# Kernel tuning notes

Hardware: AMD Instinct MI355X
Metric: run time of the kernel (lower is better)

The kernel has to match this reference:

```python
import jax, jax.numpy as jnp
import numpy as np

N, D, H = 8192, 512, 8
HD = D // H  # head_dim = 64


def setup_inputs() -> dict:
    key = jax.random.key(0)
    ks = jax.random.split(key, 9)
    s = 0.02
    return {
        "x": jax.random.normal(ks[0], (N, D), dtype=jnp.float32),
        "Wq": jax.random.normal(ks[1], (H, D, HD), dtype=jnp.float32) * s,
        "bq": jax.random.normal(ks[2], (H, HD), dtype=jnp.float32) * s,
        "Wk": jax.random.normal(ks[3], (H, D, HD), dtype=jnp.float32) * s,
        "bk": jax.random.normal(ks[4], (H, HD), dtype=jnp.float32) * s,
        "Wv": jax.random.normal(ks[5], (H, D, HD), dtype=jnp.float32) * s,
        "bv": jax.random.normal(ks[6], (H, HD), dtype=jnp.float32) * s,
        "Wo": jax.random.normal(ks[7], (D, D), dtype=jnp.float32) * s,
        "bo": jax.random.normal(ks[8], (D,), dtype=jnp.float32) * s,
    }


def reference(x, Wq, bq, Wk, bk, Wv, bv, Wo, bo):
    # Per-head linear projections (batched over heads): [H, N, HD]
    q = jnp.einsum("nd,hde->hne", x, Wq) + bq[:, None, :]
    k = jnp.einsum("nd,hde->hne", x, Wk) + bk[:, None, :]
    v = jnp.einsum("nd,hde->hne", x, Wv) + bv[:, None, :]
    scale = 1.0 / jnp.sqrt(jnp.float32(HD))
    # Global attention over all N points: scores [H, N, N]
    scores = jnp.einsum("hne,hme->hnm", q, k) * scale
    attn = jax.nn.softmax(scores, axis=-1)
    heads = jnp.einsum("hnm,hme->hne", attn, v)  # [H, N, HD]
    # Concat heads -> [N, D]
    concat = jnp.transpose(heads, (1, 0, 2)).reshape(N, D)
    out = concat @ Wo + bo
    return out + x
```

## Files before the change

kernel.cpp:

```cpp
#include <hip/hip_runtime.h>
#include <hip/hip_bf16.h>

#define NPTS 8192
#define DIM  512
#define NHEAD 8
#define HDIM 64

typedef short bf16x8 __attribute__((ext_vector_type(8)));
typedef float f32x4  __attribute__((ext_vector_type(4)));

#define GLOBAL_AS __attribute__((address_space(1)))
#define LDS_AS    __attribute__((address_space(3)))

#if __has_builtin(__builtin_amdgcn_exp2f)
#define EXP2F(x) __builtin_amdgcn_exp2f(x)
#else
#define EXP2F(x) __expf((x) * 0.6931471805599453f)
#endif

__device__ __forceinline__ unsigned short f2bf(float f) {
    union { float f; unsigned int u; } v; v.f = f;
    unsigned int r = v.u + 0x7FFFu + ((v.u >> 16) & 1u);
    return (unsigned short)(r >> 16);
}
__device__ __forceinline__ float bf2f(unsigned short u) {
    union { unsigned int i; float f; } v; v.i = ((unsigned int)u) << 16;
    return v.f;
}
__device__ __forceinline__ unsigned int pk2bf(float a, float b) {
    __hip_bfloat162 h = __float22bfloat162_rn(float2{a, b});
    union { __hip_bfloat162 h; unsigned int u; } v; v.h = h;
    return v.u;
}

__global__ __launch_bounds__(256) void cvt_x_kernel(
    const float* __restrict__ in, unsigned short* __restrict__ outp)
{
    int gid = blockIdx.x * 256 + threadIdx.x;
    float4 a = ((const float4*)in)[gid * 2];
    float4 b = ((const float4*)in)[gid * 2 + 1];
    uint4 u;
    u.x = pk2bf(a.x, a.y); u.y = pk2bf(a.z, a.w);
    u.z = pk2bf(b.x, b.y); u.w = pk2bf(b.z, b.w);
    ((uint4*)outp)[gid] = u;
}

__global__ __launch_bounds__(256) void tr_w_kernel(
    const float* __restrict__ Wq, const float* __restrict__ Wk,
    const float* __restrict__ Wv, unsigned short* __restrict__ wtq)
{
    int zh = blockIdx.z, z = zh >> 3, h = zh & 7;
    const float* src = (z == 0 ? Wq : z == 1 ? Wk : Wv) + (size_t)h * DIM * HDIM;
    unsigned short* dst = wtq + (size_t)zh * HDIM * DIM;
    int k0 = blockIdx.x * 64;
    __shared__ float tile[64][65];
    int t = threadIdx.x, c = t & 63, r = t >> 6;
    #pragma unroll
    for (int i = 0; i < 16; ++i)
        tile[r + 4 * i][c] = src[(size_t)(k0 + r + 4 * i) * HDIM + c];
    __syncthreads();
    #pragma unroll
    for (int i = 0; i < 16; ++i)
        dst[(size_t)(r + 4 * i) * DIM + k0 + c] = f2bf(tile[c][r + 4 * i]);
}

__global__ __launch_bounds__(256) void tr_wo_kernel(
    const float* __restrict__ Wo, unsigned short* __restrict__ wot)
{
    int k0 = blockIdx.x * 64, e0 = blockIdx.y * 64;
    __shared__ float tile[64][65];
    int t = threadIdx.x, c = t & 63, r = t >> 6;
    #pragma unroll
    for (int i = 0; i < 16; ++i)
        tile[r + 4 * i][c] = Wo[(size_t)(k0 + r + 4 * i) * DIM + e0 + c];
    __syncthreads();
    #pragma unroll
    for (int i = 0; i < 16; ++i)
        wot[(size_t)(e0 + r + 4 * i) * DIM + k0 + c] = f2bf(tile[c][r + 4 * i]);
}

__global__ __launch_bounds__(256) void qkv_mfma_kernel(
    const unsigned short* __restrict__ xbf,
    const unsigned short* __restrict__ wtq,
    const float* __restrict__ bq, const float* __restrict__ bk,
    const float* __restrict__ bv,
    unsigned short* __restrict__ q_bf, unsigned short* __restrict__ k_bf,
    unsigned short* __restrict__ vt_bf)
{
    const int zh = blockIdx.y, z = zh >> 3, h = zh & 7;
    const unsigned short* W = wtq + (size_t)zh * HDIM * DIM;
    const float* b = (z == 0 ? bq : z == 1 ? bk : bv) + h * HDIM;
    const int t = threadIdx.x, w = t >> 6, lane = t & 63;
    const int l15 = lane & 15, quad = lane >> 4;
    const int r0 = blockIdx.x * 128 + w * 32;

    __shared__ __align__(16) unsigned short Wlds[2][64 * 64];

    const int koff0 = l15 * 64 + (quad ^ (l15 & 7)) * 8;
    const int koff1 = koff0 ^ 32;
    const int srow   = lane >> 3;
    const int schunk = (lane & 7) ^ srow;

    const unsigned short* Wp = W + (size_t)(16 * w + srow) * DIM + schunk * 8;

    __builtin_amdgcn_global_load_lds((const GLOBAL_AS void*)Wp,
        (LDS_AS void*)&Wlds[0][(16 * w) * 64], 16, 0, 0);
    __builtin_amdgcn_global_load_lds((const GLOBAL_AS void*)(Wp + (size_t)8 * DIM),
        (LDS_AS void*)&Wlds[0][(16 * w + 8) * 64], 16, 0, 0);
    Wp += 64;
    __syncthreads();
    int buf = 0;

    f32x4 O[2][4];
    #pragma unroll
    for (int mt = 0; mt < 2; ++mt)
        #pragma unroll
        for (int tn = 0; tn < 4; ++tn) O[mt][tn] = (f32x4){0.f, 0.f, 0.f, 0.f};

    for (int k0 = 0; k0 < DIM; k0 += 64) {
        if (k0 + 64 < DIM) {
            int nb = buf ^ 1;
            __builtin_amdgcn_global_load_lds((const GLOBAL_AS void*)Wp,
                (LDS_AS void*)&Wlds[nb][(16 * w) * 64], 16, 0, 0);
            __builtin_amdgcn_global_load_lds(
                (const GLOBAL_AS void*)(Wp + (size_t)8 * DIM),
                (LDS_AS void*)&Wlds[nb][(16 * w + 8) * 64], 16, 0, 0);
            Wp += 64;
        }

        bf16x8 af[2][2];
        #pragma unroll
        for (int mt = 0; mt < 2; ++mt)
            #pragma unroll
            for (int kc = 0; kc < 2; ++kc)
                af[mt][kc] = *(const bf16x8*)
                    &xbf[(size_t)(r0 + 16 * mt + l15) * DIM + k0 + quad * 8 + 32 * kc];

        bf16x8 bf[4][2];
        #pragma unroll
        for (int tn = 0; tn < 4; ++tn) {
            bf[tn][0] = *(const bf16x8*)&Wlds[buf][1024 * tn + koff0];
            bf[tn][1] = *(const bf16x8*)&Wlds[buf][1024 * tn + koff1];
        }

        #pragma unroll
        for (int mt = 0; mt < 2; ++mt)
            #pragma unroll
            for (int tn = 0; tn < 4; ++tn) {
                O[mt][tn] = __builtin_amdgcn_mfma_f32_16x16x32_bf16(
                    af[mt][0], bf[tn][0], O[mt][tn], 0, 0, 0);
                O[mt][tn] = __builtin_amdgcn_mfma_f32_16x16x32_bf16(
                    af[mt][1], bf[tn][1], O[mt][tn], 0, 0, 0);
            }

        __syncthreads();
        buf ^= 1;
    }

    if (z < 2) {
        unsigned short* outp = (z == 0 ? q_bf : k_bf) + (size_t)h * NPTS * HDIM;
        const float sc = (z == 0) ? 0.18033688011112042f : 1.0f;
        #pragma unroll
        for (int mt = 0; mt < 2; ++mt)
            #pragma unroll
            for (int tn = 0; tn < 4; ++tn) {
                int e = l15 + 16 * tn;
                float be = b[e];
                #pragma unroll
                for (int r = 0; r < 4; ++r) {
                    int n = r0 + 16 * mt + quad * 4 + r;
                    outp[(size_t)n * HDIM + e] = f2bf((O[mt][tn][r] + be) * sc);
                }
            }
    } else {
        unsigned short* vt = vt_bf + (size_t)h * HDIM * NPTS;
        #pragma unroll
        for (int mt = 0; mt < 2; ++mt)
            #pragma unroll
            for (int tn = 0; tn < 4; ++tn) {
                int e = l15 + 16 * tn;
                float be = b[e];
                uint2 pk;
                pk.x = pk2bf(O[mt][tn][0] + be, O[mt][tn][1] + be);
                pk.y = pk2bf(O[mt][tn][2] + be, O[mt][tn][3] + be);
                *(uint2*)&vt[(size_t)e * NPTS + r0 + quad * 8 + mt * 4] = pk;
            }
    }
}

#define STAGE_TILE(B)                                                         \
    do {                                                                      \
        __builtin_amdgcn_global_load_lds((const GLOBAL_AS void*)Kp,           \
            (LDS_AS void*)&Klds[B][(16 * w) * 64], 16, 0, 0);                 \
        __builtin_amdgcn_global_load_lds((const GLOBAL_AS void*)(Kp + 8 * HDIM), \
            (LDS_AS void*)&Klds[B][(16 * w + 8) * 64], 16, 0, 0);             \
        __builtin_amdgcn_global_load_lds((const GLOBAL_AS void*)Vp0,          \
            (LDS_AS void*)&Vlds[B][(16 * w) * 64], 16, 0, 0);                 \
        __builtin_amdgcn_global_load_lds((const GLOBAL_AS void*)Vp1,          \
            (LDS_AS void*)&Vlds[B][(16 * w + 8) * 64], 16, 0, 0);             \
        Kp += 64 * HDIM; Vp0 += 64; Vp1 += 64;                                \
    } while (0)

__global__ __launch_bounds__(256) void attn_kernel(
    const unsigned short* __restrict__ qg,
    const unsigned short* __restrict__ kg,
    const unsigned short* __restrict__ vtg,
    unsigned short* __restrict__ opart,
    float* __restrict__ lpart)
{
    const int h  = blockIdx.y;
    const int ks = blockIdx.z;
    const int q0 = blockIdx.x * 256;
    const int kbase = ks * (NPTS / 2);
    const unsigned short* Q  = qg  + (size_t)h * NPTS * HDIM;
    const unsigned short* K  = kg  + (size_t)h * NPTS * HDIM;
    const unsigned short* Vt = vtg + (size_t)h * HDIM * NPTS;
    unsigned short* op = opart + (size_t)ks * NPTS * DIM;
    float* lp = lpart + (size_t)(ks * NHEAD + h) * NPTS;

    __shared__ __align__(16) unsigned short Klds[2][64 * 64];
    __shared__ __align__(16) unsigned short Vlds[2][64 * 64];

    const int t    = threadIdx.x;
    const int w    = t >> 6;
    const int lane = t & 63;
    const int l15  = lane & 15;
    const int quad = lane >> 4;

    const int koff0 = l15 * 64 + (quad ^ (l15 & 7)) * 8;
    const int koff1 = koff0 ^ 32;

    const int srow   = lane >> 3;
    const int schunk = (lane & 7) ^ srow;

    bf16x8 qf[4][2];
    #pragma unroll
    for (int m = 0; m < 4; ++m)
        #pragma unroll
        for (int kc = 0; kc < 2; ++kc)
            qf[m][kc] = *(const bf16x8*)
                &Q[(size_t)(q0 + 64 * w + 16 * m + l15) * HDIM + quad * 8 + 32 * kc];

    const bf16x8 ones = {(short)0x3F80, (short)0x3F80, (short)0x3F80,
                         (short)0x3F80, (short)0x3F80, (short)0x3F80,
                         (short)0x3F80, (short)0x3F80};
    const f32x4 Z0 = (f32x4){0.f, 0.f, 0.f, 0.f};

    f32x4 OT[4][4];
    f32x4 Lacc[4];
    #pragma unroll
    for (int te = 0; te < 4; ++te)
        #pragma unroll
        for (int m = 0; m < 4; ++m) OT[te][m] = (f32x4){0.f, 0.f, 0.f, 0.f};
    #pragma unroll
    for (int m = 0; m < 4; ++m) Lacc[m] = (f32x4){0.f, 0.f, 0.f, 0.f};

    const unsigned short* Kp  = K  + (size_t)(kbase + 16 * w + srow) * HDIM
                                   + schunk * 8;
    const unsigned short* Vp0 = Vt + (size_t)(16 * w + srow) * NPTS
                                   + kbase + schunk * 8;
    const unsigned short* Vp1 = Vp0 + (size_t)8 * NPTS;

    STAGE_TILE(0);
    __syncthreads();
    int buf = 0;

    for (int kt = 0; kt < NPTS / 2; kt += 64) {
        if (kt + 64 < NPTS / 2) {
            const int nxt = buf ^ 1;
            if (nxt) STAGE_TILE(1); else STAGE_TILE(0);
        }

        bf16x8 pt[2][4];

        {
            bf16x8 kf[2][2];
            #pragma unroll
            for (int kn = 0; kn < 2; ++kn) {
                kf[kn][0] = *(const bf16x8*)&Klds[buf][1024 * kn + koff0];
                kf[kn][1] = *(const bf16x8*)&Klds[buf][1024 * kn + koff1];
            }
            f32x4 st[2][4];
            #pragma unroll
            for (int kn = 0; kn < 2; ++kn)
                #pragma unroll
                for (int m = 0; m < 4; ++m) {
                    st[kn][m] = __builtin_amdgcn_mfma_f32_16x16x32_bf16(
                        kf[kn][0], qf[m][0], Z0, 0, 0, 0);
                    st[kn][m] = __builtin_amdgcn_mfma_f32_16x16x32_bf16(
                        kf[kn][1], qf[m][1], st[kn][m], 0, 0, 0);
                }
            #pragma unroll
            for (int m = 0; m < 4; ++m) {
                float e0 = EXP2F(st[0][m][0]);
                float e1 = EXP2F(st[0][m][1]);
                float e2 = EXP2F(st[0][m][2]);
                float e3 = EXP2F(st[0][m][3]);
                float e4 = EXP2F(st[1][m][0]);
                float e5 = EXP2F(st[1][m][1]);
                float e6 = EXP2F(st[1][m][2]);
                float e7 = EXP2F(st[1][m][3]);
                union { uint4 u; bf16x8 v; } uu;
                uu.u.x = pk2bf(e0, e1);
                uu.u.y = pk2bf(e2, e3);
                uu.u.z = pk2bf(e4, e5);
                uu.u.w = pk2bf(e6, e7);
                pt[0][m] = uu.v;
            }
        }

        bf16x8 vf0[2][2];
        #pragma unroll
        for (int te = 0; te < 2; ++te) {
            vf0[te][0] = *(const bf16x8*)&Vlds[buf][1024 * te + koff0];
            vf0[te][1] = *(const bf16x8*)&Vlds[buf][1024 * te + koff1];
        }

        {
            bf16x8 kf[2][2];
            #pragma unroll
            for (int kn = 0; kn < 2; ++kn) {
                kf[kn][0] = *(const bf16x8*)&Klds[buf][1024 * (kn + 2) + koff0];
                kf[kn][1] = *(const bf16x8*)&Klds[buf][1024 * (kn + 2) + koff1];
            }
            f32x4 st[2][4];
            #pragma unroll
            for (int kn = 0; kn < 2; ++kn)
                #pragma unroll
                for (int m = 0; m < 4; ++m) {
                    st[kn][m] = __builtin_amdgcn_mfma_f32_16x16x32_bf16(
                        kf[kn][0], qf[m][0], Z0, 0, 0, 0);
                    st[kn][m] = __builtin_amdgcn_mfma_f32_16x16x32_bf16(
                        kf[kn][1], qf[m][1], st[kn][m], 0, 0, 0);
                }
            #pragma unroll
            for (int m = 0; m < 4; ++m) {
                float e0 = EXP2F(st[0][m][0]);
                float e1 = EXP2F(st[0][m][1]);
                float e2 = EXP2F(st[0][m][2]);
                float e3 = EXP2F(st[0][m][3]);
                float e4 = EXP2F(st[1][m][0]);
                float e5 = EXP2F(st[1][m][1]);
                float e6 = EXP2F(st[1][m][2]);
                float e7 = EXP2F(st[1][m][3]);
                union { uint4 u; bf16x8 v; } uu;
                uu.u.x = pk2bf(e0, e1);
                uu.u.y = pk2bf(e2, e3);
                uu.u.z = pk2bf(e4, e5);
                uu.u.w = pk2bf(e6, e7);
                pt[1][m] = uu.v;
            }
        }

        bf16x8 vf1[2][2];
        #pragma unroll
        for (int te = 0; te < 2; ++te) {
            vf1[te][0] = *(const bf16x8*)&Vlds[buf][1024 * (te + 2) + koff0];
            vf1[te][1] = *(const bf16x8*)&Vlds[buf][1024 * (te + 2) + koff1];
        }

        #pragma unroll
        for (int kb = 0; kb < 2; ++kb)
            #pragma unroll
            for (int m = 0; m < 4; ++m)
                Lacc[m] = __builtin_amdgcn_mfma_f32_16x16x32_bf16(
                    ones, pt[kb][m], Lacc[m], 0, 0, 0);

        #pragma unroll
        for (int te = 0; te < 2; ++te)
            #pragma unroll
            for (int m = 0; m < 4; ++m) {
                OT[te][m] = __builtin_amdgcn_mfma_f32_16x16x32_bf16(
                    vf0[te][0], pt[0][m], OT[te][m], 0, 0, 0);
                OT[te][m] = __builtin_amdgcn_mfma_f32_16x16x32_bf16(
                    vf0[te][1], pt[1][m], OT[te][m], 0, 0, 0);
            }
        #pragma unroll
        for (int te = 0; te < 2; ++te)
            #pragma unroll
            for (int m = 0; m < 4; ++m) {
                OT[te + 2][m] = __builtin_amdgcn_mfma_f32_16x16x32_bf16(
                    vf1[te][0], pt[0][m], OT[te + 2][m], 0, 0, 0);
                OT[te + 2][m] = __builtin_amdgcn_mfma_f32_16x16x32_bf16(
                    vf1[te][1], pt[1][m], OT[te + 2][m], 0, 0, 0);
            }

        __syncthreads();
        buf ^= 1;
    }

    #pragma unroll
    for (int m = 0; m < 4; ++m) {
        int n = q0 + 64 * w + 16 * m + l15;
        if (quad == 0) lp[n] = Lacc[m][0];
        #pragma unroll
        for (int te = 0; te < 4; ++te) {
            uint2 pk;
            pk.x = pk2bf(OT[te][m][0], OT[te][m][1]);
            pk.y = pk2bf(OT[te][m][2], OT[te][m][3]);
            *(uint2*)&op[(size_t)n * DIM + h * HDIM + 16 * te + quad * 4] = pk;
        }
    }
}

__global__ __launch_bounds__(256) void reduce_kernel(
    unsigned short* __restrict__ op0, const unsigned short* __restrict__ op1,
    const float* __restrict__ l0, const float* __restrict__ l1)
{
    int gid = blockIdx.x * 256 + threadIdx.x;
    int n  = gid >> 7;
    int c4 = gid & 127;
    int h  = c4 >> 4;
    float inv = 1.0f / (l0[h * NPTS + n] + l1[h * NPTS + n]);
    ushort4 a = *(const ushort4*)&op0[(size_t)gid * 4];
    ushort4 b = *(const ushort4*)&op1[(size_t)gid * 4];
    uint2 o;
    o.x = pk2bf((bf2f(a.x) + bf2f(b.x)) * inv, (bf2f(a.y) + bf2f(b.y)) * inv);
    o.y = pk2bf((bf2f(a.z) + bf2f(b.z)) * inv, (bf2f(a.w) + bf2f(b.w)) * inv);
    *(uint2*)&op0[(size_t)gid * 4] = o;
}

__global__ __launch_bounds__(256) void out_mfma_kernel(
    const unsigned short* __restrict__ cc,
    const unsigned short* __restrict__ wot,
    const float* __restrict__ bo, const float* __restrict__ x,
    float* __restrict__ outp)
{
    const int t = threadIdx.x, w = t >> 6, lane = t & 63;
    const int l15 = lane & 15, quad = lane >> 4;
    const int r0 = blockIdx.x * 128 + w * 32;
    const int c0 = blockIdx.y * 64;

    f32x4 O[2][4];
    #pragma unroll
    for (int mt = 0; mt < 2; ++mt)
        #pragma unroll
        for (int tn = 0; tn < 4; ++tn) O[mt][tn] = (f32x4){0.f, 0.f, 0.f, 0.f};

    for (int k0 = 0; k0 < DIM; k0 += 64) {
        bf16x8 af[2][2], bf[4][2];
        #pragma unroll
        for (int mt = 0; mt < 2; ++mt)
            #pragma unroll
            for (int kc = 0; kc < 2; ++kc)
                af[mt][kc] = *(const bf16x8*)
                    &cc[(size_t)(r0 + 16 * mt + l15) * DIM + k0 + quad * 8 + 32 * kc];
        #pragma unroll
        for (int tn = 0; tn < 4; ++tn)
            #pragma unroll
            for (int kc = 0; kc < 2; ++kc)
                bf[tn][kc] = *(const bf16x8*)
                    &wot[(size_t)(c0 + l15 + 16 * tn) * DIM + k0 + quad * 8 + 32 * kc];
        #pragma unroll
        for (int mt = 0; mt < 2; ++mt)
            #pragma unroll
            for (int tn = 0; tn < 4; ++tn) {
                O[mt][tn] = __builtin_amdgcn_mfma_f32_16x16x32_bf16(
                    af[mt][0], bf[tn][0], O[mt][tn], 0, 0, 0);
                O[mt][tn] = __builtin_amdgcn_mfma_f32_16x16x32_bf16(
                    af[mt][1], bf[tn][1], O[mt][tn], 0, 0, 0);
            }
    }

    #pragma unroll
    for (int mt = 0; mt < 2; ++mt)
        #pragma unroll
        for (int tn = 0; tn < 4; ++tn) {
            int e = c0 + l15 + 16 * tn;
            float be = bo[e];
            #pragma unroll
            for (int r = 0; r < 4; ++r) {
                int n = r0 + 16 * mt + quad * 4 + r;
                outp[(size_t)n * DIM + e] = O[mt][tn][r] + be + x[(size_t)n * DIM + e];
            }
        }
}

extern "C" void kernel_launch(void* const* d_in, const int* in_sizes, int n_in,
                              void* d_out, int out_size, void* d_ws, size_t ws_size,
                              hipStream_t stream) {
    const float* x  = (const float*)d_in[0];
    const float* Wq = (const float*)d_in[1];
    const float* bq = (const float*)d_in[2];
    const float* Wk = (const float*)d_in[3];
    const float* bk = (const float*)d_in[4];
    const float* Wv = (const float*)d_in[5];
    const float* bv = (const float*)d_in[6];
    const float* Wo = (const float*)d_in[7];
    const float* bo = (const float*)d_in[8];
    float* out = (float*)d_out;

    const size_t per = (size_t)NHEAD * NPTS * HDIM;
    unsigned short* xbf   = (unsigned short*)d_ws;
    unsigned short* wtq   = xbf + (size_t)NPTS * DIM;
    unsigned short* wot   = wtq + (size_t)24 * HDIM * DIM;
    unsigned short* q_bf  = wot + (size_t)DIM * DIM;
    unsigned short* k_bf  = q_bf + per;
    unsigned short* vt_bf = k_bf + per;
    unsigned short* op0   = vt_bf + per;
    unsigned short* op1   = op0 + (size_t)NPTS * DIM;
    float*          lpart = (float*)(op1 + (size_t)NPTS * DIM);

    cvt_x_kernel<<<dim3(NPTS * DIM / 8 / 256), 256, 0, stream>>>(x, xbf);
    tr_w_kernel<<<dim3(8, 1, 24), 256, 0, stream>>>(Wq, Wk, Wv, wtq);
    tr_wo_kernel<<<dim3(8, 8), 256, 0, stream>>>(Wo, wot);
    qkv_mfma_kernel<<<dim3(NPTS / 128, 24), 256, 0, stream>>>(
        xbf, wtq, bq, bk, bv, q_bf, k_bf, vt_bf);
    attn_kernel<<<dim3(NPTS / 256, NHEAD, 2), 256, 0, stream>>>(
        q_bf, k_bf, vt_bf, op0, lpart);
    reduce_kernel<<<dim3(NPTS * DIM / 4 / 256), 256, 0, stream>>>(
        op0, op1, lpart, lpart + (size_t)NHEAD * NPTS);
    out_mfma_kernel<<<dim3(NPTS / 128, DIM / 64), 256, 0, stream>>>(
        op0, wot, bo, x, out);
}
```

Baseline: 295.8 us.

## Fuse split-KV reduction into output projection and stage Wo tiles in LDS

Removes the separate reduce kernel that merged the two split-KV partial outputs and normalized by the softmax denominators. The output projection kernel now loads both partials, runs MFMAs on each into a per-head temporary, and scales by 1/(l0+l1) before accumulating. This works because each 64-wide k-block corresponds to one head. Wo tiles are also double-buffered into swizzled LDS via global_load_lds instead of read directly from global memory by every wave. In exchange the MFMA count in the projection doubles, and op0/op1 are each read 8 times across column blocks.

```diff
diff --git a/kernel.cpp b/kernel.cpp
--- a/kernel.cpp
+++ b/kernel.cpp
@@ -403,25 +403,11 @@
     }
 }
 
-__global__ __launch_bounds__(256) void reduce_kernel(
-    unsigned short* __restrict__ op0, const unsigned short* __restrict__ op1,
-    const float* __restrict__ l0, const float* __restrict__ l1)
-{
-    int gid = blockIdx.x * 256 + threadIdx.x;
-    int n  = gid >> 7;
-    int c4 = gid & 127;
-    int h  = c4 >> 4;
-    float inv = 1.0f / (l0[h * NPTS + n] + l1[h * NPTS + n]);
-    ushort4 a = *(const ushort4*)&op0[(size_t)gid * 4];
-    ushort4 b = *(const ushort4*)&op1[(size_t)gid * 4];
-    uint2 o;
-    o.x = pk2bf((bf2f(a.x) + bf2f(b.x)) * inv, (bf2f(a.y) + bf2f(b.y)) * inv);
-    o.y = pk2bf((bf2f(a.z) + bf2f(b.z)) * inv, (bf2f(a.w) + bf2f(b.w)) * inv);
-    *(uint2*)&op0[(size_t)gid * 4] = o;
-}
-
 __global__ __launch_bounds__(256) void out_mfma_kernel(
-    const unsigned short* __restrict__ cc,
+    const unsigned short* __restrict__ op0,
+    const unsigned short* __restrict__ op1,
+    const float* __restrict__ l0,
+    const float* __restrict__ l1,
     const unsigned short* __restrict__ wot,
     const float* __restrict__ bo, const float* __restrict__ x,
     float* __restrict__ outp)
@@ -431,6 +417,25 @@
     const int r0 = blockIdx.x * 128 + w * 32;
     const int c0 = blockIdx.y * 64;
 
+    __shared__ __align__(16) unsigned short Wlds[2][64 * 64];
+
+    const int koff0 = l15 * 64 + (quad ^ (l15 & 7)) * 8;
+    const int koff1 = koff0 ^ 32;
+    const int srow   = lane >> 3;
+    const int schunk = (lane & 7) ^ srow;
+
+    const f32x4 Z0 = (f32x4){0.f, 0.f, 0.f, 0.f};
+
+    const unsigned short* Wp = wot + (size_t)(c0 + 16 * w + srow) * DIM
+                                   + schunk * 8;
+    __builtin_amdgcn_global_load_lds((const GLOBAL_AS void*)Wp,
+        (LDS_AS void*)&Wlds[0][(16 * w) * 64], 16, 0, 0);
+    __builtin_amdgcn_global_load_lds((const GLOBAL_AS void*)(Wp + (size_t)8 * DIM),
+        (LDS_AS void*)&Wlds[0][(16 * w + 8) * 64], 16, 0, 0);
+    Wp += 64;
+    __syncthreads();
+    int buf = 0;
+
     f32x4 O[2][4];
     #pragma unroll
     for (int mt = 0; mt < 2; ++mt)
@@ -438,28 +443,69 @@
         for (int tn = 0; tn < 4; ++tn) O[mt][tn] = (f32x4){0.f, 0.f, 0.f, 0.f};
 
     for (int k0 = 0; k0 < DIM; k0 += 64) {
-        bf16x8 af[2][2], bf[4][2];
+        const int h = k0 >> 6;
+        if (k0 + 64 < DIM) {
+            int nb = buf ^ 1;
+            __builtin_amdgcn_global_load_lds((const GLOBAL_AS void*)Wp,
+                (LDS_AS void*)&Wlds[nb][(16 * w) * 64], 16, 0, 0);
+            __builtin_amdgcn_global_load_lds(
+                (const GLOBAL_AS void*)(Wp + (size_t)8 * DIM),
+                (LDS_AS void*)&Wlds[nb][(16 * w + 8) * 64], 16, 0, 0);
+            Wp += 64;
+        }
+
+        bf16x8 af0[2][2], af1[2][2];
         #pragma unroll
         for (int mt = 0; mt < 2; ++mt)
             #pragma unroll
-            for (int kc = 0; kc < 2; ++kc)
-                af[mt][kc] = *(const bf16x8*)
-                    &cc[(size_t)(r0 + 16 * mt + l15) * DIM + k0 + quad * 8 + 32 * kc];
-        #pragma unroll
-        for (int tn = 0; tn < 4; ++tn)
-            #pragma unroll
-            for (int kc = 0; kc < 2; ++kc)
-                bf[tn][kc] = *(const bf16x8*)
-                    &wot[(size_t)(c0 + l15 + 16 * tn) * DIM + k0 + quad * 8 + 32 * kc];
-        #pragma unroll
-        for (int mt = 0; mt < 2; ++mt)
+            for (int kc = 0; kc < 2; ++kc) {
+                size_t idx = (size_t)(r0 + 16 * mt + l15) * DIM
+                             + k0 + quad * 8 + 32 * kc;
+                af0[mt][kc] = *(const bf16x8*)&op0[idx];
+                af1[mt][kc] = *(const bf16x8*)&op1[idx];
+            }
+
+        float inv0[4], inv1[4];
+        {
+            const float4 a0 = *(const float4*)&l0[(size_t)h * NPTS + r0 + quad * 4];
+            const float4 b0 = *(const float4*)&l1[(size_t)h * NPTS + r0 + quad * 4];
+            const float4 a1 = *(const float4*)&l0[(size_t)h * NPTS + r0 + 16 + quad * 4];
+            const float4 b1 = *(const float4*)&l1[(size_t)h * NPTS + r0 + 16 + quad * 4];
+            inv0[0] = 1.0f / (a0.x + b0.x); inv0[1] = 1.0f / (a0.y + b0.y);
+            inv0[2] = 1.0f / (a0.z + b0.z); inv0[3] = 1.0f / (a0.w + b0.w);
+            inv1[0] = 1.0f / (a1.x + b1.x); inv1[1] = 1.0f / (a1.y + b1.y);
+            inv1[2] = 1.0f / (a1.z + b1.z); inv1[3] = 1.0f / (a1.w + b1.w);
+        }
+
+        bf16x8 bf[4][2];
+        #pragma unroll
+        for (int tn = 0; tn < 4; ++tn) {
+            bf[tn][0] = *(const bf16x8*)&Wlds[buf][1024 * tn + koff0];
+            bf[tn][1] = *(const bf16x8*)&Wlds[buf][1024 * tn + koff1];
+        }
+
+        #pragma unroll
+        for (int mt = 0; mt < 2; ++mt) {
+            const float* inv = (mt == 0) ? inv0 : inv1;
             #pragma unroll
             for (int tn = 0; tn < 4; ++tn) {
-                O[mt][tn] = __builtin_amdgcn_mfma_f32_16x16x32_bf16(
-                    af[mt][0], bf[tn][0], O[mt][tn], 0, 0, 0);
-                O[mt][tn] = __builtin_amdgcn_mfma_f32_16x16x32_bf16(
-                    af[mt][1], bf[tn][1], O[mt][tn], 0, 0, 0);
-            }
+                f32x4 Os;
+                Os = __builtin_amdgcn_mfma_f32_16x16x32_bf16(
+                    af0[mt][0], bf[tn][0], Z0, 0, 0, 0);
+                Os = __builtin_amdgcn_mfma_f32_16x16x32_bf16(
+                    af0[mt][1], bf[tn][1], Os, 0, 0, 0);
+                Os = __builtin_amdgcn_mfma_f32_16x16x32_bf16(
+                    af1[mt][0], bf[tn][0], Os, 0, 0, 0);
+                Os = __builtin_amdgcn_mfma_f32_16x16x32_bf16(
+                    af1[mt][1], bf[tn][1], Os, 0, 0, 0);
+                #pragma unroll
+                for (int r = 0; r < 4; ++r)
+                    O[mt][tn][r] += Os[r] * inv[r];
+            }
+        }
+
+        __syncthreads();
+        buf ^= 1;
     }
 
     #pragma unroll
@@ -508,8 +554,6 @@
         xbf, wtq, bq, bk, bv, q_bf, k_bf, vt_bf);
     attn_kernel<<<dim3(NPTS / 256, NHEAD, 2), 256, 0, stream>>>(
         q_bf, k_bf, vt_bf, op0, lpart);
-    reduce_kernel<<<dim3(NPTS * DIM / 4 / 256), 256, 0, stream>>>(
-        op0, op1, lpart, lpart + (size_t)NHEAD * NPTS);
     out_mfma_kernel<<<dim3(NPTS / 128, DIM / 64), 256, 0, stream>>>(
-        op0, wot, bo, x, out);
-}
+        op0, op1, lpart, lpart + (size_t)NHEAD * NPTS, wot, bo, x, out);
+}
```

New measurement: 289.0 us. 2.3% less time.
